# Performance work log

Measured on AMD Instinct MI355X. Metric: run time of the kernel, lower is better.

## Reference

```python
import jax, jax.numpy as jnp
import numpy as np

B, C, H, W = 16, 512, 48, 48
INTER = 64  # C // reduction


def setup_inputs() -> dict:
    key = jax.random.key(0)
    k1, k2, k3, k4, k5 = jax.random.split(key, 5)
    s = 0.05
    return {
        "x": jax.random.normal(k1, (B, C, H, W), dtype=jnp.float32),
        "Wq": jax.random.normal(k2, (INTER, C), dtype=jnp.float32) * s,
        "Wk": jax.random.normal(k3, (INTER, C), dtype=jnp.float32) * s,
        "Wv": jax.random.normal(k4, (C, C), dtype=jnp.float32) * s,
        "gamma": jax.random.normal(k5, (1,), dtype=jnp.float32),
    }


def reference(x, Wq, Wk, Wv, gamma):
    b, c, h, w = x.shape
    n = h * w
    xf = x.reshape(b, c, n)                       # (B, C, N)
    # 1x1 convs == channel-mixing GEMMs
    q = jnp.einsum("ic,bcn->bin", Wq, xf)         # (B, inter, N)
    k = jnp.einsum("ic,bcn->bin", Wk, xf)         # (B, inter, N)
    v = jnp.einsum("oc,bcn->bon", Wv, xf)         # (B, C, N)
    # attn[b, n, m] = q[b, :, n] . k[b, :, m]; softmax over m
    attn = jnp.einsum("bin,bim->bnm", q, k)       # (B, N, N)
    attn = jax.nn.softmax(attn, axis=-1)
    # out[b, c, n] = sum_m v[b, c, m] * attn[b, n, m]
    out = jnp.einsum("bcm,bnm->bcn", v, attn).reshape(b, c, h, w)
    return gamma[0] * out + x
```

## Files before the change

kernel.cpp:

```cpp
#include <hip/hip_runtime.h>

#define BATCH 16
#define CHN   512
#define INTER 64
#define NPIX  2304

typedef _Float16 f16;
typedef _Float16 f16x8 __attribute__((ext_vector_type(8)));
typedef _Float16 f16x4 __attribute__((ext_vector_type(4)));
typedef short    s16x8 __attribute__((ext_vector_type(8)));
typedef float    f32x16 __attribute__((ext_vector_type(16)));

#define XT_OFF   ((size_t)0)
#define QT_OFF   ((size_t)37748736)
#define KT_OFF   ((size_t)42467328)
#define VB_OFF   ((size_t)47185920)
#define WHQ_OFF  ((size_t)84934656)
#define WHK_OFF  ((size_t)85000192)
#define WHV_OFF  ((size_t)85065728)

#define LOG2E 1.4426950408889634f

__device__ inline unsigned short f2bf(float f) {
    unsigned int u = __float_as_uint(f);
    unsigned int r = (u + 0x7FFFu + ((u >> 16) & 1u)) >> 16;
    return (unsigned short)r;
}

__device__ inline unsigned pack_bf16(float a, float b) {
    unsigned ua = __float_as_uint(a) + 0x8000u;
    unsigned ub = __float_as_uint(b) + 0x8000u;
    return __builtin_amdgcn_perm(ub, ua, 0x07060302u);
}

__device__ inline unsigned pack_f16(float a, float b) {
    f16 ha = (f16)a, hb = (f16)b;
    unsigned short ua = *(unsigned short*)&ha, ub = *(unsigned short*)&hb;
    return (unsigned)ua | ((unsigned)ub << 16);
}

__device__ inline float exp2_fast(float x) {
#if __has_builtin(__builtin_amdgcn_exp2f)
    return __builtin_amdgcn_exp2f(x);
#else
    float r; asm("v_exp_f32 %0, %1" : "=v"(r) : "v"(x)); return r;
#endif
}

__device__ inline void gload_lds16(const void* g, void* l) {
    __builtin_amdgcn_global_load_lds(
        (const __attribute__((address_space(1))) void*)g,
        (__attribute__((address_space(3))) void*)l, 16, 0, 0);
}

__device__ inline void swap32(unsigned x, unsigned y, unsigned& nx, unsigned& ny, int lh) {
#if __has_builtin(__builtin_amdgcn_permlane32_swap)
    auto r = __builtin_amdgcn_permlane32_swap(x, y, false, false);
    nx = r[0]; ny = r[1];
#else
    const unsigned xs = (unsigned)__shfl_xor((int)x, 32, 64);
    const unsigned ys = (unsigned)__shfl_xor((int)y, 32, 64);
    nx = lh ? ys : x;
    ny = lh ? y  : xs;
#endif
}

__global__ __launch_bounds__(256) void convert_x_kernel(
    const float* __restrict__ x, f16* __restrict__ xT)
{
    const int n0 = blockIdx.x * 64;
    const int c0 = blockIdx.y * 64;
    const int b  = blockIdx.z;
    const int t  = threadIdx.x;

    __shared__ float tile[64][65];

    {
        const int cr   = t >> 2;
        const int ncol = (t & 3) * 16;
        const float* src = x + ((size_t)b * CHN + (size_t)(c0 + cr)) * NPIX + n0 + ncol;
        #pragma unroll
        for (int u = 0; u < 4; ++u) {
            const float4 v4 = *(const float4*)(src + u * 4);
            tile[cr][ncol + u * 4 + 0] = v4.x;
            tile[cr][ncol + u * 4 + 1] = v4.y;
            tile[cr][ncol + u * 4 + 2] = v4.z;
            tile[cr][ncol + u * 4 + 3] = v4.w;
        }
    }
    __syncthreads();
    #pragma unroll
    for (int r = 0; r < 2; ++r) {
        const int id = t + r * 256;
        const int n  = id >> 3;
        const int cg = id & 7;
        f16x8 o;
        #pragma unroll
        for (int j = 0; j < 8; ++j) o[j] = (f16)tile[cg * 8 + j][n];
        *(f16x8*)(xT + ((size_t)b * NPIX + (size_t)(n0 + n)) * CHN + c0 + cg * 8) = o;
    }
}

__global__ __launch_bounds__(256) void convert_w_kernel(
    const float* __restrict__ Wq, const float* __restrict__ Wk,
    const float* __restrict__ Wv, f16* __restrict__ whq,
    f16* __restrict__ whk, f16* __restrict__ whv)
{
    const int which = blockIdx.y;
    const float* src; f16* dst; int count;
    if (which == 0)      { src = Wq; dst = whq; count = 64 * 512; }
    else if (which == 1) { src = Wk; dst = whk; count = 64 * 512; }
    else                 { src = Wv; dst = whv; count = 512 * 512; }
    const int i = (blockIdx.x * 256 + threadIdx.x) * 4;
    if (i < count) {
        const float4 v4 = *(const float4*)(src + i);
        f16x4 o;
        o[0] = (f16)v4.x; o[1] = (f16)v4.y; o[2] = (f16)v4.z; o[3] = (f16)v4.w;
        *(f16x4*)(dst + i) = o;
    }
}

__global__ __launch_bounds__(256, 2) void proj_kernel(
    const f16* __restrict__ xT, const f16* __restrict__ whq,
    const f16* __restrict__ whk, const f16* __restrict__ whv,
    f16* __restrict__ qTo, f16* __restrict__ kTo,
    unsigned short* __restrict__ vout)
{
    const int nt = blockIdx.x;
    const int rt = blockIdx.y;
    const int b  = blockIdx.z;
    const int t  = threadIdx.x;
    const int wave = t >> 6, lane = t & 63;
    const int row = lane & 31, lh = lane >> 5;

    __shared__ f16 smem[2 * 128 * 72];
    f16 (*wsm)[72] = (f16(*)[72])smem;
    f16 (*xs)[72]  = (f16(*)[72])(smem + 128 * 72);

    f32x16 acc[4];
    #pragma unroll
    for (int s = 0; s < 4; ++s)
        #pragma unroll
        for (int r = 0; r < 16; ++r) acc[s][r] = 0.0f;

    for (int c0 = 0; c0 < CHN; c0 += 64) {
        __syncthreads();
        #pragma unroll
        for (int r = 0; r < 4; ++r) {
            const int id = t + r * 256;
            const int co = id >> 3, cg = id & 7;
            const f16* src;
            if (rt == 0) src = (co < 64) ? (whq + (size_t)co * CHN)
                                         : (whk + (size_t)(co - 64) * CHN);
            else         src = whv + (size_t)((rt - 1) * 128 + co) * CHN;
            *(f16x8*)&wsm[co][cg * 8] = *(const f16x8*)(src + c0 + cg * 8);
        }
        #pragma unroll
        for (int r = 0; r < 4; ++r) {
            const int id = t + r * 256;
            const int n = id >> 3, cg = id & 7;
            *(f16x8*)&xs[n][cg * 8] =
                *(const f16x8*)(xT + ((size_t)b * NPIX + (size_t)(nt * 128 + n)) * CHN + c0 + cg * 8);
        }
        __syncthreads();

        #pragma unroll
        for (int kk = 0; kk < 64; kk += 16) {
            const f16x8 bf = *(const f16x8*)&xs[wave * 32 + row][kk + lh * 8];
            #pragma unroll
            for (int cs = 0; cs < 4; ++cs) {
                const f16x8 af = *(const f16x8*)&wsm[cs * 32 + row][kk + lh * 8];
                acc[cs] = __builtin_amdgcn_mfma_f32_32x32x16_f16(af, bf, acc[cs], 0, 0, 0);
            }
        }
    }

    __syncthreads();
    unsigned short* eb = (unsigned short*)smem;
    const int nl = wave * 32 + row;

    if (rt == 0) {
        #pragma unroll
        for (int cs = 0; cs < 4; ++cs) {
            const float sc = (cs < 2) ? LOG2E : 1.0f;
            #pragma unroll
            for (int tp = 0; tp < 8; ++tp) {
                const int r = tp * 2;
                const int i = cs * 32 + (r & 3) + 8 * (r >> 2) + 4 * lh;
                *(unsigned*)&eb[nl * 130 + i] =
                    pack_f16(acc[cs][r] * sc, acc[cs][r + 1] * sc);
            }
        }
    } else {
        #pragma unroll
        for (int cs = 0; cs < 4; ++cs)
            #pragma unroll
            for (int r = 0; r < 16; ++r) {
                const int cl = cs * 32 + (r & 3) + 8 * (r >> 2) + 4 * lh;
                eb[cl * 130 + nl] = f2bf(acc[cs][r]);
            }
    }
    __syncthreads();

    #pragma unroll
    for (int u = 0; u < 8; ++u) {
        const int id = t + u * 256;
        const int rr = id >> 4;
        const int ch = id & 15;
        const unsigned short* src = &eb[rr * 130 + ch * 8];
        s16x8 w;
        #pragma unroll
        for (int k = 0; k < 4; ++k)
            ((unsigned*)&w)[k] = *(const unsigned*)(src + k * 2);
        if (rt == 0) {
            f16* dst = (ch < 8)
                ? (qTo + ((size_t)b * NPIX + nt * 128 + rr) * INTER + ch * 8)
                : (kTo + ((size_t)b * NPIX + nt * 128 + rr) * INTER + (ch - 8) * 8);
            *(s16x8*)dst = w;
        } else {
            *(s16x8*)(vout + ((size_t)b * CHN + (size_t)((rt - 1) * 128 + rr)) * NPIX
                      + nt * 128 + ch * 8) = w;
        }
    }
}

__global__ __launch_bounds__(256, 3) void attn_kernel(
    const float* __restrict__ x, const float* __restrict__ gamma,
    const f16* __restrict__ qT, const f16* __restrict__ kT,
    const unsigned short* __restrict__ vglob, float* __restrict__ out)
{
    const int nt = blockIdx.x;
    const int cq = blockIdx.y;
    const int b  = blockIdx.z;
    const int t  = threadIdx.x;
    const int wave = t >> 6, lane = t & 63;
    const int row = lane & 31, lh = lane >> 5;

    __shared__ short vbuf[2][128 * 64];
    __shared__ f16   kbuf[64 * 64];

    const unsigned short* vq = vglob + ((size_t)b * CHN + (size_t)cq * 128) * NPIX;
    const f16* kb = kT + (size_t)b * NPIX * INTER;

    const int lrow = lane >> 3;
    const int lch  = lane & 7;

    const int xorv = row & 7;

    f16x8 qf[4];
    {
        const f16* qrow = qT + ((size_t)b * NPIX
                          + (size_t)(nt * 128 + wave * 32 + row)) * INTER + lh * 8;
        #pragma unroll
        for (int k0 = 0; k0 < 4; ++k0) qf[k0] = *(const f16x8*)(qrow + k0 * 16);
    }

    #pragma unroll
    for (int j = 0; j < 4; ++j) {
        const int r = j * 32 + wave * 8 + lrow;
        gload_lds16(vq + (size_t)r * NPIX + ((lch ^ (r & 7)) * 8),
                    &vbuf[0][(j * 32 + wave * 8) * 64]);
    }
    #pragma unroll
    for (int j = 0; j < 2; ++j) {
        const int r = j * 32 + wave * 8 + lrow;
        gload_lds16(kb + (size_t)r * INTER + ((lch ^ (r & 7)) * 8),
                    &kbuf[(j * 32 + wave * 8) * 64]);
    }
    __syncthreads();

    f32x16 accv[4];
    #pragma unroll
    for (int s = 0; s < 4; ++s)
        #pragma unroll
        for (int r = 0; r < 16; ++r) accv[s][r] = 0.0f;

    float lrun = 0.0f;
    union PB { unsigned u[4]; s16x8 v; };

    for (int it = 0; it < NPIX / 64; ++it) {
        const int cur = it & 1, nxt = cur ^ 1;
        const int m1 = (it < NPIX / 64 - 1) ? (it + 1) * 64 : 0;

        #pragma unroll
        for (int j = 0; j < 4; ++j) {
            const int r = j * 32 + wave * 8 + lrow;
            gload_lds16(vq + (size_t)r * NPIX + m1 + ((lch ^ (r & 7)) * 8),
                        &vbuf[nxt][(j * 32 + wave * 8) * 64]);
        }

        union PB pb[4];
        #pragma unroll
        for (int mh = 0; mh < 2; ++mh) {
            f32x16 sacc;
            #pragma unroll
            for (int r = 0; r < 16; ++r) sacc[r] = 0.0f;
            #pragma unroll
            for (int k0 = 0; k0 < 4; ++k0) {
                const f16x8 af = *(const f16x8*)&kbuf[(mh * 32 + row) * 64
                                    + (((k0 * 2 + lh) ^ xorv) * 8)];
                sacc = __builtin_amdgcn_mfma_f32_32x32x16_f16(af, qf[k0], sacc, 0, 0, 0);
            }
            float lp = 0.0f;
            unsigned pg[8];
            #pragma unroll
            for (int tt = 0; tt < 8; ++tt) {
                const float p0 = exp2_fast(sacc[2 * tt + 0]);
                const float p1 = exp2_fast(sacc[2 * tt + 1]);
                lp += p0 + p1;
                pg[tt] = pack_bf16(p0, p1);
            }
            lrun += lp;
            #pragma unroll
            for (int half = 0; half < 2; ++half)
                #pragma unroll
                for (int p = 0; p < 2; ++p) {
                    unsigned nx, ny;
                    swap32(pg[half * 4 + p], pg[half * 4 + 2 + p], nx, ny, lh);
                    pb[2 * mh + half].u[p]     = nx;
                    pb[2 * mh + half].u[p + 2] = ny;
                }
        }

        __syncthreads();

        #pragma unroll
        for (int j = 0; j < 2; ++j) {
            const int r = j * 32 + wave * 8 + lrow;
            gload_lds16(kb + (size_t)(m1 + r) * INTER + ((lch ^ (r & 7)) * 8),
                        &kbuf[(j * 32 + wave * 8) * 64]);
        }

        #pragma unroll
        for (int cs = 0; cs < 4; ++cs)
            #pragma unroll
            for (int kk = 0; kk < 4; ++kk) {
                const s16x8 va = *(const s16x8*)&vbuf[cur][(cs * 32 + row) * 64
                                    + (((kk * 2 + lh) ^ xorv) * 8)];
                accv[cs] = __builtin_amdgcn_mfma_f32_32x32x16_bf16(
                    va, pb[kk].v, accv[cs], 0, 0, 0);
            }

        __syncthreads();
    }

    const float g = gamma[0];
    const float linv = 1.0f / (lrun + __shfl_xor(lrun, 32, 64));
    const int n = nt * 128 + wave * 32 + row;

    #pragma unroll
    for (int cs = 0; cs < 4; ++cs)
        #pragma unroll
        for (int r = 0; r < 16; ++r) {
            const int c = cq * 128 + cs * 32 + (r & 3) + 8 * (r >> 2) + 4 * lh;
            const size_t idx = ((size_t)b * CHN + c) * NPIX + n;
            out[idx] = g * accv[cs][r] * linv + x[idx];
        }
}

extern "C" void kernel_launch(void* const* d_in, const int* in_sizes, int n_in,
                              void* d_out, int out_size, void* d_ws, size_t ws_size,
                              hipStream_t stream) {
    (void)in_sizes; (void)n_in; (void)out_size; (void)ws_size;
    const float* x     = (const float*)d_in[0];
    const float* Wq    = (const float*)d_in[1];
    const float* Wk    = (const float*)d_in[2];
    const float* Wv    = (const float*)d_in[3];
    const float* gamma = (const float*)d_in[4];
    float* out = (float*)d_out;
    char* ws = (char*)d_ws;

    f16* xT  = (f16*)(ws + XT_OFF);
    f16* qTp = (f16*)(ws + QT_OFF);
    f16* kTp = (f16*)(ws + KT_OFF);
    unsigned short* vb = (unsigned short*)(ws + VB_OFF);
    f16* whq = (f16*)(ws + WHQ_OFF);
    f16* whk = (f16*)(ws + WHK_OFF);
    f16* whv = (f16*)(ws + WHV_OFF);

    convert_x_kernel<<<dim3(36, 8, 16), 256, 0, stream>>>(x, xT);
    convert_w_kernel<<<dim3(256, 3, 1), 256, 0, stream>>>(Wq, Wk, Wv, whq, whk, whv);
    proj_kernel<<<dim3(18, 5, 16), 256, 0, stream>>>(xT, whq, whk, whv, qTp, kTp, vb);
    attn_kernel<<<dim3(18, 4, 16), 256, 0, stream>>>(x, gamma, qTp, kTp, vb, out);
}
```

Measured before the change: 351.8 us.

## Fuse fp32-to-fp16 conversion into projection and widen attention channel tile

Removes the separate x-transpose and weight-conversion kernels: the projection kernel now reads fp32 x and weights directly, converting to fp16 in registers and transposing x through an LDS staging tile. Separately, the attention kernel now processes 256 channels per block instead of 128, halving the grid and the number of times Q·K scores and softmax are recomputed per pixel tile. The costs are more LDS and accumulator registers (occupancy hint lowered from 3 to 2) and fewer blocks in the attention grid. The projection also re-reads fp32 x from global memory across five row-tile blocks instead of reading half-size fp16 data.

```diff
diff --git a/kernel.cpp b/kernel.cpp
--- a/kernel.cpp
+++ b/kernel.cpp
@@ -11,13 +11,9 @@
 typedef short    s16x8 __attribute__((ext_vector_type(8)));
 typedef float    f32x16 __attribute__((ext_vector_type(16)));
 
-#define XT_OFF   ((size_t)0)
 #define QT_OFF   ((size_t)37748736)
 #define KT_OFF   ((size_t)42467328)
 #define VB_OFF   ((size_t)47185920)
-#define WHQ_OFF  ((size_t)84934656)
-#define WHK_OFF  ((size_t)85000192)
-#define WHV_OFF  ((size_t)85065728)
 
 #define LOG2E 1.4426950408889634f
 
@@ -65,64 +61,9 @@
 #endif
 }
 
-__global__ __launch_bounds__(256) void convert_x_kernel(
-    const float* __restrict__ x, f16* __restrict__ xT)
-{
-    const int n0 = blockIdx.x * 64;
-    const int c0 = blockIdx.y * 64;
-    const int b  = blockIdx.z;
-    const int t  = threadIdx.x;
-
-    __shared__ float tile[64][65];
-
-    {
-        const int cr   = t >> 2;
-        const int ncol = (t & 3) * 16;
-        const float* src = x + ((size_t)b * CHN + (size_t)(c0 + cr)) * NPIX + n0 + ncol;
-        #pragma unroll
-        for (int u = 0; u < 4; ++u) {
-            const float4 v4 = *(const float4*)(src + u * 4);
-            tile[cr][ncol + u * 4 + 0] = v4.x;
-            tile[cr][ncol + u * 4 + 1] = v4.y;
-            tile[cr][ncol + u * 4 + 2] = v4.z;
-            tile[cr][ncol + u * 4 + 3] = v4.w;
-        }
-    }
-    __syncthreads();
-    #pragma unroll
-    for (int r = 0; r < 2; ++r) {
-        const int id = t + r * 256;
-        const int n  = id >> 3;
-        const int cg = id & 7;
-        f16x8 o;
-        #pragma unroll
-        for (int j = 0; j < 8; ++j) o[j] = (f16)tile[cg * 8 + j][n];
-        *(f16x8*)(xT + ((size_t)b * NPIX + (size_t)(n0 + n)) * CHN + c0 + cg * 8) = o;
-    }
-}
-
-__global__ __launch_bounds__(256) void convert_w_kernel(
-    const float* __restrict__ Wq, const float* __restrict__ Wk,
-    const float* __restrict__ Wv, f16* __restrict__ whq,
-    f16* __restrict__ whk, f16* __restrict__ whv)
-{
-    const int which = blockIdx.y;
-    const float* src; f16* dst; int count;
-    if (which == 0)      { src = Wq; dst = whq; count = 64 * 512; }
-    else if (which == 1) { src = Wk; dst = whk; count = 64 * 512; }
-    else                 { src = Wv; dst = whv; count = 512 * 512; }
-    const int i = (blockIdx.x * 256 + threadIdx.x) * 4;
-    if (i < count) {
-        const float4 v4 = *(const float4*)(src + i);
-        f16x4 o;
-        o[0] = (f16)v4.x; o[1] = (f16)v4.y; o[2] = (f16)v4.z; o[3] = (f16)v4.w;
-        *(f16x4*)(dst + i) = o;
-    }
-}
-
 __global__ __launch_bounds__(256, 2) void proj_kernel(
-    const f16* __restrict__ xT, const f16* __restrict__ whq,
-    const f16* __restrict__ whk, const f16* __restrict__ whv,
+    const float* __restrict__ x, const float* __restrict__ Wq,
+    const float* __restrict__ Wk, const float* __restrict__ Wv,
     f16* __restrict__ qTo, f16* __restrict__ kTo,
     unsigned short* __restrict__ vout)
 {
@@ -134,6 +75,7 @@
     const int row = lane & 31, lh = lane >> 5;
 
     __shared__ f16 smem[2 * 128 * 72];
+    __shared__ float xstage[64][129];
     f16 (*wsm)[72] = (f16(*)[72])smem;
     f16 (*xs)[72]  = (f16(*)[72])(smem + 128 * 72);
 
@@ -145,22 +87,46 @@
 
     for (int c0 = 0; c0 < CHN; c0 += 64) {
         __syncthreads();
-        #pragma unroll
-        for (int r = 0; r < 4; ++r) {
-            const int id = t + r * 256;
-            const int co = id >> 3, cg = id & 7;
-            const f16* src;
-            if (rt == 0) src = (co < 64) ? (whq + (size_t)co * CHN)
-                                         : (whk + (size_t)(co - 64) * CHN);
-            else         src = whv + (size_t)((rt - 1) * 128 + co) * CHN;
-            *(f16x8*)&wsm[co][cg * 8] = *(const f16x8*)(src + c0 + cg * 8);
-        }
+
+        {
+            const int wr = t >> 4;
+            const int fq = t & 15;
+            #pragma unroll
+            for (int rr = 0; rr < 8; ++rr) {
+                const int ro = rr * 16 + wr;
+                const float* src;
+                if (rt == 0) src = (ro < 64) ? (Wq + (size_t)ro * CHN)
+                                             : (Wk + (size_t)(ro - 64) * CHN);
+                else         src = Wv + (size_t)((rt - 1) * 128 + ro) * CHN;
+                const float4 v4 = *(const float4*)(src + c0 + fq * 4);
+                f16x4 o;
+                o[0] = (f16)v4.x; o[1] = (f16)v4.y; o[2] = (f16)v4.z; o[3] = (f16)v4.w;
+                *(f16x4*)&wsm[ro][fq * 4] = o;
+            }
+        }
+        {
+            const int cr = t >> 2;
+            const int nq = (t & 3) * 32;
+            const float* src = x + ((size_t)b * CHN + (size_t)(c0 + cr)) * NPIX
+                               + nt * 128 + nq;
+            #pragma unroll
+            for (int u = 0; u < 8; ++u) {
+                const float4 v4 = *(const float4*)(src + u * 4);
+                xstage[cr][nq + u * 4 + 0] = v4.x;
+                xstage[cr][nq + u * 4 + 1] = v4.y;
+                xstage[cr][nq + u * 4 + 2] = v4.z;
+                xstage[cr][nq + u * 4 + 3] = v4.w;
+            }
+        }
+        __syncthreads();
         #pragma unroll
         for (int r = 0; r < 4; ++r) {
             const int id = t + r * 256;
             const int n = id >> 3, cg = id & 7;
-            *(f16x8*)&xs[n][cg * 8] =
-                *(const f16x8*)(xT + ((size_t)b * NPIX + (size_t)(nt * 128 + n)) * CHN + c0 + cg * 8);
+            f16x8 o;
+            #pragma unroll
+            for (int j = 0; j < 8; ++j) o[j] = (f16)xstage[cg * 8 + j][n];
+            *(f16x8*)&xs[n][cg * 8] = o;
         }
         __syncthreads();
 
@@ -224,7 +190,7 @@
     }
 }
 
-__global__ __launch_bounds__(256, 3) void attn_kernel(
+__global__ __launch_bounds__(256, 2) void attn_kernel(
     const float* __restrict__ x, const float* __restrict__ gamma,
     const f16* __restrict__ qT, const f16* __restrict__ kT,
     const unsigned short* __restrict__ vglob, float* __restrict__ out)
@@ -236,10 +202,10 @@
     const int wave = t >> 6, lane = t & 63;
     const int row = lane & 31, lh = lane >> 5;
 
-    __shared__ short vbuf[2][128 * 64];
+    __shared__ short vbuf[2][256 * 64];
     __shared__ f16   kbuf[64 * 64];
 
-    const unsigned short* vq = vglob + ((size_t)b * CHN + (size_t)cq * 128) * NPIX;
+    const unsigned short* vq = vglob + ((size_t)b * CHN + (size_t)cq * 256) * NPIX;
     const f16* kb = kT + (size_t)b * NPIX * INTER;
 
     const int lrow = lane >> 3;
@@ -256,7 +222,7 @@
     }
 
     #pragma unroll
-    for (int j = 0; j < 4; ++j) {
+    for (int j = 0; j < 8; ++j) {
         const int r = j * 32 + wave * 8 + lrow;
         gload_lds16(vq + (size_t)r * NPIX + ((lch ^ (r & 7)) * 8),
                     &vbuf[0][(j * 32 + wave * 8) * 64]);
@@ -269,9 +235,9 @@
     }
     __syncthreads();
 
-    f32x16 accv[4];
-    #pragma unroll
-    for (int s = 0; s < 4; ++s)
+    f32x16 accv[8];
+    #pragma unroll
+    for (int s = 0; s < 8; ++s)
         #pragma unroll
         for (int r = 0; r < 16; ++r) accv[s][r] = 0.0f;
 
@@ -283,7 +249,7 @@
         const int m1 = (it < NPIX / 64 - 1) ? (it + 1) * 64 : 0;
 
         #pragma unroll
-        for (int j = 0; j < 4; ++j) {
+        for (int j = 0; j < 8; ++j) {
             const int r = j * 32 + wave * 8 + lrow;
             gload_lds16(vq + (size_t)r * NPIX + m1 + ((lch ^ (r & 7)) * 8),
                         &vbuf[nxt][(j * 32 + wave * 8) * 64]);
@@ -332,7 +298,7 @@
         }
 
         #pragma unroll
-        for (int cs = 0; cs < 4; ++cs)
+        for (int cs = 0; cs < 8; ++cs)
             #pragma unroll
             for (int kk = 0; kk < 4; ++kk) {
                 const s16x8 va = *(const s16x8*)&vbuf[cur][(cs * 32 + row) * 64
@@ -349,10 +315,10 @@
     const int n = nt * 128 + wave * 32 + row;
 
     #pragma unroll
-    for (int cs = 0; cs < 4; ++cs)
+    for (int cs = 0; cs < 8; ++cs)
         #pragma unroll
         for (int r = 0; r < 16; ++r) {
-            const int c = cq * 128 + cs * 32 + (r & 3) + 8 * (r >> 2) + 4 * lh;
+            const int c = cq * 256 + cs * 32 + (r & 3) + 8 * (r >> 2) + 4 * lh;
             const size_t idx = ((size_t)b * CHN + c) * NPIX + n;
             out[idx] = g * accv[cs][r] * linv + x[idx];
         }
@@ -370,16 +336,10 @@
     float* out = (float*)d_out;
     char* ws = (char*)d_ws;
 
-    f16* xT  = (f16*)(ws + XT_OFF);
     f16* qTp = (f16*)(ws + QT_OFF);
     f16* kTp = (f16*)(ws + KT_OFF);
     unsigned short* vb = (unsigned short*)(ws + VB_OFF);
-    f16* whq = (f16*)(ws + WHQ_OFF);
-    f16* whk = (f16*)(ws + WHK_OFF);
-    f16* whv = (f16*)(ws + WHV_OFF);
-
-    convert_x_kernel<<<dim3(36, 8, 16), 256, 0, stream>>>(x, xT);
-    convert_w_kernel<<<dim3(256, 3, 1), 256, 0, stream>>>(Wq, Wk, Wv, whq, whk, whv);
-    proj_kernel<<<dim3(18, 5, 16), 256, 0, stream>>>(xT, whq, whk, whv, qTp, kTp, vb);
-    attn_kernel<<<dim3(18, 4, 16), 256, 0, stream>>>(x, gamma, qTp, kTp, vb, out);
-}
+
+    proj_kernel<<<dim3(18, 5, 16), 256, 0, stream>>>(x, Wq, Wk, Wv, qTp, kTp, vb);
+    attn_kernel<<<dim3(18, 2, 16), 256, 0, stream>>>(x, gamma, qTp, kTp, vb, out);
+}
```

Result: slower. 379.0 us (+7.7%).
